# Performance work log

Measured on AMD Instinct MI355X. Metric: run time of the kernel, lower is better.

Reference implementation:

```python
import jax, jax.numpy as jnp
import numpy as np

AUDIO_IN = VIDEO_IN = TEXT_IN = 300
AH = VH = TH = 100
POST_DIM = 300
OUT_DIM = 300
BATCH = 128


def setup_inputs() -> dict:
    key = jax.random.key(0)
    ks = jax.random.split(key, 12)
    s = lambda fan_in: 1.0 / np.sqrt(fan_in)
    fusion_dim = (AH + 1) * (VH + 1) * (TH + 1)
    return {
        "audio_x": jax.random.normal(ks[0], (BATCH, AUDIO_IN), jnp.float32),
        "video_x": jax.random.normal(ks[1], (BATCH, VIDEO_IN), jnp.float32),
        "text_x": jax.random.normal(ks[2], (BATCH, TEXT_IN), jnp.float32),
        "Wa": jax.random.normal(ks[3], (AH, AUDIO_IN), jnp.float32) * s(AUDIO_IN),
        "ba": jnp.zeros((AH,), jnp.float32),
        "Wv": jax.random.normal(ks[4], (VH, VIDEO_IN), jnp.float32) * s(VIDEO_IN),
        "bv": jnp.zeros((VH,), jnp.float32),
        "Wt": jax.random.normal(ks[5], (TH, TEXT_IN), jnp.float32) * s(TEXT_IN),
        "bt": jnp.zeros((TH,), jnp.float32),
        "W1": jax.random.normal(ks[6], (POST_DIM, fusion_dim), jnp.float32) * s(fusion_dim),
        "b1": jnp.zeros((POST_DIM,), jnp.float32),
        "W2": jax.random.normal(ks[7], (OUT_DIM, POST_DIM), jnp.float32) * s(POST_DIM),
        "b2": jnp.zeros((OUT_DIM,), jnp.float32),
    }


def reference(audio_x, video_x, text_x, Wa, ba, Wv, bv, Wt, bt, W1, b1, W2, b2):
    B = audio_x.shape[0]
    audio_h = audio_x @ Wa.T + ba          # [B, AH]
    video_h = video_x @ Wv.T + bv          # [B, VH]
    text_h = text_x @ Wt.T + bt            # [B, TH]
    ones = jnp.ones((B, 1), audio_h.dtype)
    _a = jnp.concatenate([ones, audio_h], axis=1)   # [B, AH+1]
    _v = jnp.concatenate([ones, video_h], axis=1)   # [B, VH+1]
    _t = jnp.concatenate([ones, text_h], axis=1)    # [B, TH+1]
    # three-way outer product; flatten order matches torch bmm chain: (a, v, t)
    fusion = jnp.einsum('ba,bv,bt->bavt', _a, _v, _t).reshape(B, -1)
    # dropout is identity in eval mode
    h = jax.nn.relu(fusion @ W1.T + b1)
    out = jax.nn.relu(h @ W2.T + b2)
    return out
```

## Files before the change

### kernel.cpp

```cpp
#include <hip/hip_runtime.h>
#include <hip/hip_bf16.h>
#include <stdint.h>

#define NB      128
#define NH      101
#define NIN     300
#define NP      300
#define NO      300
#define K_TOT   1030301
#define NAV     10201
#define CHUNK   32
#define NCHUNKS ((K_TOT + CHUNK - 1) / CHUNK)
#define RANGES_DEFAULT 153
#define PTILES  5
#define PPAD    320
#define ASTRIDE 40
#define TSTRIDE 102

typedef __attribute__((ext_vector_type(8))) short bf16x8;
typedef __attribute__((ext_vector_type(4))) float f32x4;

static __device__ __forceinline__ unsigned short f2bf(float f) {
    union { float f; unsigned u; } x; x.f = f;
    unsigned r = x.u + 0x7fffu + ((x.u >> 16) & 1u);
    return (unsigned short)(r >> 16);
}
static __device__ __forceinline__ float bf2f(unsigned short h) {
    union { unsigned u; float f; } x; x.u = ((unsigned)h) << 16;
    return x.f;
}

__global__ __launch_bounds__(256) void proj_kernel(
    const float* __restrict__ ax, const float* __restrict__ vx, const float* __restrict__ tx,
    const float* __restrict__ Wa, const float* __restrict__ ba,
    const float* __restrict__ Wv, const float* __restrict__ bv,
    const float* __restrict__ Wt, const float* __restrict__ bt,
    float* __restrict__ Af, float* __restrict__ Vf, float* __restrict__ Tf)
{
    int g = blockIdx.x * 256 + threadIdx.x;
    if (g >= 3 * NB * NH) return;
    int mod = g / (NB * NH);
    int rem = g - mod * (NB * NH);
    int b = rem / NH, j = rem - b * NH;
    const float* x = (mod == 0) ? ax : (mod == 1) ? vx : tx;
    const float* W = (mod == 0) ? Wa : (mod == 1) ? Wv : Wt;
    const float* bi = (mod == 0) ? ba : (mod == 1) ? bv : bt;
    float val;
    if (j == 0) {
        val = 1.0f;
    } else {
        const float4* xr = (const float4*)(x + (size_t)b * NIN);
        const float4* wr = (const float4*)(W + (size_t)(j - 1) * NIN);
        float s0 = 0.f, s1 = 0.f, s2 = 0.f, s3 = 0.f;
        #pragma unroll 5
        for (int i = 0; i < NIN / 4; ++i) {
            float4 a = xr[i], w = wr[i];
            s0 += a.x * w.x; s1 += a.y * w.y; s2 += a.z * w.z; s3 += a.w * w.w;
        }
        val = (s0 + s1) + (s2 + s3) + bi[j - 1];
    }
    float* dst = (mod == 0) ? Af : (mod == 1) ? Vf : Tf;
    dst[b * NH + j] = val;
}

__global__ __launch_bounds__(256) void av_kernel(
    const float* __restrict__ Af, const float* __restrict__ Vf, const float* __restrict__ Tf,
    unsigned short* __restrict__ AVbf, unsigned short* __restrict__ Tbf)
{
    int g = blockIdx.x * 256 + threadIdx.x;
    if (g < NB * TSTRIDE) {
        int b = g / TSTRIDE, j = g - b * TSTRIDE;
        Tbf[g] = (j < NH) ? f2bf(Tf[b * NH + j]) : (unsigned short)0;
    }
    if (g < NAV * NB) {
        int av = g >> 7, b = g & 127;
        int a = av / NH, v = av - a * NH;
        AVbf[g] = f2bf(Af[b * NH + a] * Vf[b * NH + v]);
    }
}

__global__ __launch_bounds__(256) void fusion_gemm_kernel(
    const float* __restrict__ W1, const unsigned short* __restrict__ AVbf,
    const unsigned short* __restrict__ Tbf, float* __restrict__ partial, int cpr)
{
    __shared__ unsigned short Tl[NB * TSTRIDE];
    __shared__ unsigned short Al[NB * ASTRIDE];
    __shared__ unsigned short Wl[64 * ASTRIDE];

    const int tid   = threadIdx.x;
    const int ptile = blockIdx.x;
    const int rng   = blockIdx.y;
    const int wave  = tid >> 6;
    const int lane  = tid & 63;
    const int ln15  = lane & 15;
    const int quad  = lane >> 4;

    {
        const unsigned* src = (const unsigned*)Tbf;
        unsigned* dst = (unsigned*)Tl;
        for (int i = tid; i < NB * TSTRIDE / 2; i += 256) dst[i] = src[i];
    }

    const int c0 = rng * cpr;
    const int c1 = min(c0 + cpr, NCHUNKS);

    const int kk   = tid & 31;
    const int bg   = (tid >> 5) << 4;
    const int wrow = tid >> 5;

    f32x4 acc[8];
    #pragma unroll
    for (int i = 0; i < 8; ++i) acc[i] = (f32x4){0.f, 0.f, 0.f, 0.f};

    float    wreg[8];
    unsigned avp[8];
    unsigned tt = 0;
    bool     valid = true;

    __syncthreads();

    auto issue_loads = [&](int c) {
        unsigned kg = (unsigned)c * CHUNK + (unsigned)kk;
        valid = (kg < K_TOT);
        unsigned kc = valid ? kg : (unsigned)(K_TOT - 1);
        #pragma unroll
        for (int it = 0; it < 8; ++it) {
            int pr = ptile * 64 + wrow + it * 8;
            if (pr > NP - 1) pr = NP - 1;
            wreg[it] = W1[(size_t)pr * K_TOT + kc];
        }
        unsigned av = kc / 101u;
        tt = kc - av * 101u;
        const unsigned* avsrc = (const unsigned*)(AVbf + (size_t)av * NB + bg);
        #pragma unroll
        for (int j = 0; j < 8; ++j) avp[j] = avsrc[j];
    };

    if (c0 < c1) issue_loads(c0);

    for (int c = c0; c < c1; ++c) {
        #pragma unroll
        for (int it = 0; it < 8; ++it)
            Wl[(wrow + it * 8) * ASTRIDE + kk] = f2bf(wreg[it]);
        #pragma unroll
        for (int j2 = 0; j2 < 8; ++j2) {
            unsigned pk = avp[j2];
            int b0 = bg + j2 * 2;
            float a0 = bf2f((unsigned short)(pk & 0xffffu));
            float a1 = bf2f((unsigned short)(pk >> 16));
            float t0 = bf2f(Tl[b0 * TSTRIDE + tt]);
            float t1 = bf2f(Tl[(b0 + 1) * TSTRIDE + tt]);
            Al[b0 * ASTRIDE + kk]       = valid ? f2bf(a0 * t0) : (unsigned short)0;
            Al[(b0 + 1) * ASTRIDE + kk] = valid ? f2bf(a1 * t1) : (unsigned short)0;
        }
        __syncthreads();
        if (c + 1 < c1) issue_loads(c + 1);
        bf16x8 bfrag = *(const bf16x8*)&Wl[(wave * 16 + ln15) * ASTRIDE + quad * 8];
        #pragma unroll
        for (int bt = 0; bt < 8; ++bt) {
            bf16x8 afrag = *(const bf16x8*)&Al[(bt * 16 + ln15) * ASTRIDE + quad * 8];
            acc[bt] = __builtin_amdgcn_mfma_f32_16x16x32_bf16(afrag, bfrag, acc[bt], 0, 0, 0);
        }
        __syncthreads();
    }

    const int p = ptile * 64 + wave * 16 + ln15;
    #pragma unroll
    for (int bt = 0; bt < 8; ++bt) {
        #pragma unroll
        for (int rg = 0; rg < 4; ++rg) {
            int b = bt * 16 + quad * 4 + rg;
            partial[((size_t)rng * NB + b) * PPAD + p] = acc[bt][rg];
        }
    }
}

__global__ __launch_bounds__(256) void reduce_kernel(
    const float* __restrict__ partial, const float* __restrict__ b1,
    float* __restrict__ h, int R)
{
    int g = blockIdx.x * 256 + threadIdx.x;
    if (g >= NB * NP) return;
    int b = g / NP, p = g - b * NP;
    float s = b1[p];
    const float* src = partial + (size_t)b * PPAD + p;
    for (int r = 0; r < R; ++r) s += src[(size_t)r * NB * PPAD];
    h[b * NP + p] = fmaxf(s, 0.f);
}

__global__ __launch_bounds__(256) void gemm2_kernel(
    const float* __restrict__ h, const float* __restrict__ W2,
    const float* __restrict__ b2, float* __restrict__ out)
{
    int g = blockIdx.x * 256 + threadIdx.x;
    if (g >= NB * NO) return;
    int b = g / NO, o = g - b * NO;
    const float4* hr = (const float4*)(h + (size_t)b * NP);
    const float4* wr = (const float4*)(W2 + (size_t)o * NP);
    float s0 = 0.f, s1 = 0.f, s2 = 0.f, s3 = 0.f;
    #pragma unroll 5
    for (int i = 0; i < NP / 4; ++i) {
        float4 a = hr[i], w = wr[i];
        s0 += a.x * w.x; s1 += a.y * w.y; s2 += a.z * w.z; s3 += a.w * w.w;
    }
    out[g] = fmaxf((s0 + s1) + (s2 + s3) + b2[o], 0.f);
}

extern "C" void kernel_launch(void* const* d_in, const int* in_sizes, int n_in,
                              void* d_out, int out_size, void* d_ws, size_t ws_size,
                              hipStream_t stream) {
    const float* ax = (const float*)d_in[0];
    const float* vx = (const float*)d_in[1];
    const float* tx = (const float*)d_in[2];
    const float* Wa = (const float*)d_in[3];
    const float* ba = (const float*)d_in[4];
    const float* Wv = (const float*)d_in[5];
    const float* bv = (const float*)d_in[6];
    const float* Wt = (const float*)d_in[7];
    const float* bt = (const float*)d_in[8];
    const float* W1 = (const float*)d_in[9];
    const float* b1 = (const float*)d_in[10];
    const float* W2 = (const float*)d_in[11];
    const float* b2 = (const float*)d_in[12];
    float* out = (float*)d_out;

    char* ws = (char*)d_ws;
    size_t off = 0;
    float* Af = (float*)(ws + off); off += (size_t)NB * NH * 4;
    float* Vf = (float*)(ws + off); off += (size_t)NB * NH * 4;
    float* Tf = (float*)(ws + off); off += (size_t)NB * NH * 4;
    float* h  = (float*)(ws + off); off += (size_t)NB * NP * 4;
    unsigned short* Tbf  = (unsigned short*)(ws + off); off += (size_t)NB * TSTRIDE * 2;
    unsigned short* AVbf = (unsigned short*)(ws + off); off += (size_t)NAV * NB * 2;
    size_t fixed = off;
    const size_t per_range = (size_t)NB * PPAD * 4;
    int R = RANGES_DEFAULT;
    if (ws_size < fixed + (size_t)R * per_range) {
        size_t avail = (ws_size > fixed) ? (ws_size - fixed) : per_range;
        R = (int)(avail / per_range);
        if (R < 1) R = 1;
    }
    float* partial = (float*)(ws + fixed);
    int cpr = (NCHUNKS + R - 1) / R;

    proj_kernel<<<(3 * NB * NH + 255) / 256, 256, 0, stream>>>(
        ax, vx, tx, Wa, ba, Wv, bv, Wt, bt, Af, Vf, Tf);
    av_kernel<<<(NAV * NB + 255) / 256, 256, 0, stream>>>(Af, Vf, Tf, AVbf, Tbf);
    fusion_gemm_kernel<<<dim3(PTILES, R), 256, 0, stream>>>(W1, AVbf, Tbf, partial, cpr);
    reduce_kernel<<<(NB * NP + 255) / 256, 256, 0, stream>>>(partial, b1, h, R);
    gemm2_kernel<<<(NB * NO + 255) / 256, 256, 0, stream>>>(h, W2, b2, out);
}
```

Measured before the change: 1.762 ms.

## Restructure fusion GEMM to iterate over av pairs with register-built MFMA fragments

The fusion GEMM now splits K by (a,v) pairs instead of flat 32-wide chunks. Each wave loads its W1 row segment of 101 t-values directly into registers as float4 and converts with a packed bf16 instruction. The A fragment is built on the fly from the LDS-resident T table scaled by the av scalar, so the per-chunk LDS staging of W and A and both barriers go away. The cost is padding waste in the final 5-element slice of each segment, misaligned float4 loads of W1 since rows are 101 floats apart, and the workspace-size fallback being dropped.

```diff
diff --git a/kernel.cpp b/kernel.cpp
--- a/kernel.cpp
+++ b/kernel.cpp
@@ -9,13 +9,11 @@
 #define NO      300
 #define K_TOT   1030301
 #define NAV     10201
-#define CHUNK   32
-#define NCHUNKS ((K_TOT + CHUNK - 1) / CHUNK)
-#define RANGES_DEFAULT 153
+#define TSTR    104
+#define PPAD    320
 #define PTILES  5
-#define PPAD    320
-#define ASTRIDE 40
-#define TSTRIDE 102
+#define RANGES  153
+#define APR     ((NAV + RANGES - 1) / RANGES)
 
 typedef __attribute__((ext_vector_type(8))) short bf16x8;
 typedef __attribute__((ext_vector_type(4))) float f32x4;
@@ -28,6 +26,17 @@
 static __device__ __forceinline__ float bf2f(unsigned short h) {
     union { unsigned u; float f; } x; x.u = ((unsigned)h) << 16;
     return x.f;
+}
+static __device__ __forceinline__ float u2f(uint32_t u) {
+    union { uint32_t u; float f; } x; x.u = u; return x.f;
+}
+static __device__ __forceinline__ uint32_t pk2(float x, float y) {
+    uint32_t r;
+    asm("v_cvt_pk_bf16_f32 %0, %1, %2" : "=v"(r) : "v"(x), "v"(y));
+    return r;
+}
+static __device__ __forceinline__ float4 loadf4(const float* q) {
+    float4 v; __builtin_memcpy(&v, q, 16); return v;
 }
 
 __global__ __launch_bounds__(256) void proj_kernel(
@@ -68,8 +77,8 @@
     unsigned short* __restrict__ AVbf, unsigned short* __restrict__ Tbf)
 {
     int g = blockIdx.x * 256 + threadIdx.x;
-    if (g < NB * TSTRIDE) {
-        int b = g / TSTRIDE, j = g - b * TSTRIDE;
+    if (g < NB * TSTR) {
+        int b = g / TSTR, j = g - b * TSTR;
         Tbf[g] = (j < NH) ? f2bf(Tf[b * NH + j]) : (unsigned short)0;
     }
     if (g < NAV * NB) {
@@ -79,89 +88,114 @@
     }
 }
 
-__global__ __launch_bounds__(256) void fusion_gemm_kernel(
+__global__ __launch_bounds__(256, 3) void fusion_gemm_kernel(
     const float* __restrict__ W1, const unsigned short* __restrict__ AVbf,
-    const unsigned short* __restrict__ Tbf, float* __restrict__ partial, int cpr)
-{
-    __shared__ unsigned short Tl[NB * TSTRIDE];
-    __shared__ unsigned short Al[NB * ASTRIDE];
-    __shared__ unsigned short Wl[64 * ASTRIDE];
-
-    const int tid   = threadIdx.x;
+    const unsigned short* __restrict__ Tbf, float* __restrict__ partial, int apr)
+{
+    __shared__ __align__(16) unsigned short Tl[NB * TSTR];
+    __shared__ __align__(16) unsigned short AVl[(APR + 1) * NB];
+
+    const int tid  = threadIdx.x;
     const int ptile = blockIdx.x;
-    const int rng   = blockIdx.y;
-    const int wave  = tid >> 6;
-    const int lane  = tid & 63;
-    const int ln15  = lane & 15;
-    const int quad  = lane >> 4;
+    const int rng  = blockIdx.y;
+    const int wave = tid >> 6;
+    const int lane = tid & 63;
+    const int ln15 = lane & 15;
+    const int quad = lane >> 4;
+
+    const int av0 = rng * apr;
+    const int av_end = min(av0 + apr, NAV);
+    const int nav = av_end - av0;
 
     {
-        const unsigned* src = (const unsigned*)Tbf;
-        unsigned* dst = (unsigned*)Tl;
-        for (int i = tid; i < NB * TSTRIDE / 2; i += 256) dst[i] = src[i];
-    }
-
-    const int c0 = rng * cpr;
-    const int c1 = min(c0 + cpr, NCHUNKS);
-
-    const int kk   = tid & 31;
-    const int bg   = (tid >> 5) << 4;
-    const int wrow = tid >> 5;
+        const uint32_t* src = (const uint32_t*)Tbf;
+        uint32_t* dst = (uint32_t*)Tl;
+        #pragma unroll
+        for (int i = 0; i < (NB * TSTR / 2) / 256; ++i)
+            dst[i * 256 + tid] = src[i * 256 + tid];
+        if (nav > 0) {
+            const uint32_t* s2 = (const uint32_t*)(AVbf + (size_t)av0 * NB);
+            uint32_t* d2 = (uint32_t*)AVl;
+            const int ndw = nav * (NB / 2);
+            for (int i = tid; i < ndw; i += 256) d2[i] = s2[i];
+        }
+    }
+    __syncthreads();
+
+    int prow = ptile * 64 + wave * 16 + ln15;
+    if (prow > NP - 1) prow = NP - 1;
+    const float* wrow = W1 + (size_t)prow * K_TOT;
 
     f32x4 acc[8];
     #pragma unroll
     for (int i = 0; i < 8; ++i) acc[i] = (f32x4){0.f, 0.f, 0.f, 0.f};
 
-    float    wreg[8];
-    unsigned avp[8];
-    unsigned tt = 0;
-    bool     valid = true;
-
-    __syncthreads();
-
-    auto issue_loads = [&](int c) {
-        unsigned kg = (unsigned)c * CHUNK + (unsigned)kk;
-        valid = (kg < K_TOT);
-        unsigned kc = valid ? kg : (unsigned)(K_TOT - 1);
-        #pragma unroll
-        for (int it = 0; it < 8; ++it) {
-            int pr = ptile * 64 + wrow + it * 8;
-            if (pr > NP - 1) pr = NP - 1;
-            wreg[it] = W1[(size_t)pr * K_TOT + kc];
-        }
-        unsigned av = kc / 101u;
-        tt = kc - av * 101u;
-        const unsigned* avsrc = (const unsigned*)(AVbf + (size_t)av * NB + bg);
-        #pragma unroll
-        for (int j = 0; j < 8; ++j) avp[j] = avsrc[j];
-    };
-
-    if (c0 < c1) issue_loads(c0);
-
-    for (int c = c0; c < c1; ++c) {
-        #pragma unroll
-        for (int it = 0; it < 8; ++it)
-            Wl[(wrow + it * 8) * ASTRIDE + kk] = f2bf(wreg[it]);
-        #pragma unroll
-        for (int j2 = 0; j2 < 8; ++j2) {
-            unsigned pk = avp[j2];
-            int b0 = bg + j2 * 2;
-            float a0 = bf2f((unsigned short)(pk & 0xffffu));
-            float a1 = bf2f((unsigned short)(pk >> 16));
-            float t0 = bf2f(Tl[b0 * TSTRIDE + tt]);
-            float t1 = bf2f(Tl[(b0 + 1) * TSTRIDE + tt]);
-            Al[b0 * ASTRIDE + kk]       = valid ? f2bf(a0 * t0) : (unsigned short)0;
-            Al[(b0 + 1) * ASTRIDE + kk] = valid ? f2bf(a1 * t1) : (unsigned short)0;
-        }
-        __syncthreads();
-        if (c + 1 < c1) issue_loads(c + 1);
-        bf16x8 bfrag = *(const bf16x8*)&Wl[(wave * 16 + ln15) * ASTRIDE + quad * 8];
-        #pragma unroll
-        for (int bt = 0; bt < 8; ++bt) {
-            bf16x8 afrag = *(const bf16x8*)&Al[(bt * 16 + ln15) * ASTRIDE + quad * 8];
-            acc[bt] = __builtin_amdgcn_mfma_f32_16x16x32_bf16(afrag, bfrag, acc[bt], 0, 0, 0);
-        }
-        __syncthreads();
+    #pragma unroll 1
+    for (int a = 0; a < nav; ++a) {
+        const float* wbase = wrow + (size_t)(av0 + a) * 101;
+
+        float4 wq[6];
+        #pragma unroll
+        for (int s = 0; s < 3; ++s) {
+            const float* q = wbase + s * 32 + quad * 8;
+            wq[s * 2]     = loadf4(q);
+            wq[s * 2 + 1] = loadf4(q + 4);
+        }
+        float w3[5];
+        #pragma unroll
+        for (int j = 0; j < 5; ++j) w3[j] = wbase[96 + j];
+
+        float avf[8];
+        #pragma unroll
+        for (int bt = 0; bt < 8; ++bt)
+            avf[bt] = bf2f(AVl[a * NB + bt * 16 + ln15]);
+
+        #pragma unroll
+        for (int s = 0; s < 3; ++s) {
+            union { bf16x8 v; uint32_t u[4]; } bf;
+            bf.u[0] = pk2(wq[s * 2].x,     wq[s * 2].y);
+            bf.u[1] = pk2(wq[s * 2].z,     wq[s * 2].w);
+            bf.u[2] = pk2(wq[s * 2 + 1].x, wq[s * 2 + 1].y);
+            bf.u[3] = pk2(wq[s * 2 + 1].z, wq[s * 2 + 1].w);
+            #pragma unroll
+            for (int bt = 0; bt < 8; ++bt) {
+                const uint4 t4 = *(const uint4*)&Tl[(bt * 16 + ln15) * TSTR + s * 32 + quad * 8];
+                const float s0 = avf[bt];
+                union { bf16x8 v; uint32_t u[4]; } af;
+                af.u[0] = pk2(s0 * u2f(t4.x << 16), s0 * u2f(t4.x & 0xffff0000u));
+                af.u[1] = pk2(s0 * u2f(t4.y << 16), s0 * u2f(t4.y & 0xffff0000u));
+                af.u[2] = pk2(s0 * u2f(t4.z << 16), s0 * u2f(t4.z & 0xffff0000u));
+                af.u[3] = pk2(s0 * u2f(t4.w << 16), s0 * u2f(t4.w & 0xffff0000u));
+                acc[bt] = __builtin_amdgcn_mfma_f32_16x16x32_bf16(af.v, bf.v, acc[bt], 0, 0, 0);
+            }
+        }
+
+        {
+            union { bf16x8 v; uint32_t u[4]; } bf;
+            if (quad == 0) {
+                bf.u[0] = pk2(w3[0], w3[1]);
+                bf.u[1] = pk2(w3[2], w3[3]);
+                bf.u[2] = pk2(w3[4], 0.f);
+                bf.u[3] = 0u;
+            } else {
+                bf.u[0] = 0u; bf.u[1] = 0u; bf.u[2] = 0u; bf.u[3] = 0u;
+            }
+            #pragma unroll
+            for (int bt = 0; bt < 8; ++bt) {
+                union { bf16x8 v; uint32_t u[4]; } af;
+                if (quad == 0) {
+                    const uint4 t4 = *(const uint4*)&Tl[(bt * 16 + ln15) * TSTR + 96];
+                    const float s0 = avf[bt];
+                    af.u[0] = pk2(s0 * u2f(t4.x << 16), s0 * u2f(t4.x & 0xffff0000u));
+                    af.u[1] = pk2(s0 * u2f(t4.y << 16), s0 * u2f(t4.y & 0xffff0000u));
+                    af.u[2] = pk2(s0 * u2f(t4.z << 16), s0 * u2f(t4.z & 0xffff0000u));
+                    af.u[3] = pk2(s0 * u2f(t4.w << 16), s0 * u2f(t4.w & 0xffff0000u));
+                } else {
+                    af.u[0] = 0u; af.u[1] = 0u; af.u[2] = 0u; af.u[3] = 0u;
+                }
+                acc[bt] = __builtin_amdgcn_mfma_f32_16x16x32_bf16(af.v, bf.v, acc[bt], 0, 0, 0);
+            }
+        }
     }
 
     const int p = ptile * 64 + wave * 16 + ln15;
@@ -230,23 +264,17 @@
     float* Vf = (float*)(ws + off); off += (size_t)NB * NH * 4;
     float* Tf = (float*)(ws + off); off += (size_t)NB * NH * 4;
     float* h  = (float*)(ws + off); off += (size_t)NB * NP * 4;
-    unsigned short* Tbf  = (unsigned short*)(ws + off); off += (size_t)NB * TSTRIDE * 2;
+    unsigned short* Tbf  = (unsigned short*)(ws + off); off += (size_t)NB * TSTR * 2;
     unsigned short* AVbf = (unsigned short*)(ws + off); off += (size_t)NAV * NB * 2;
-    size_t fixed = off;
-    const size_t per_range = (size_t)NB * PPAD * 4;
-    int R = RANGES_DEFAULT;
-    if (ws_size < fixed + (size_t)R * per_range) {
-        size_t avail = (ws_size > fixed) ? (ws_size - fixed) : per_range;
-        R = (int)(avail / per_range);
-        if (R < 1) R = 1;
-    }
-    float* partial = (float*)(ws + fixed);
-    int cpr = (NCHUNKS + R - 1) / R;
+    float* partial = (float*)(ws + off);
+
+    const int R = RANGES;
+    const int apr = APR;
 
     proj_kernel<<<(3 * NB * NH + 255) / 256, 256, 0, stream>>>(
         ax, vx, tx, Wa, ba, Wv, bv, Wt, bt, Af, Vf, Tf);
     av_kernel<<<(NAV * NB + 255) / 256, 256, 0, stream>>>(Af, Vf, Tf, AVbf, Tbf);
-    fusion_gemm_kernel<<<dim3(PTILES, R), 256, 0, stream>>>(W1, AVbf, Tbf, partial, cpr);
+    fusion_gemm_kernel<<<dim3(PTILES, R), 256, 0, stream>>>(W1, AVbf, Tbf, partial, apr);
     reduce_kernel<<<(NB * NP + 255) / 256, 256, 0, stream>>>(partial, b1, h, R);
     gemm2_kernel<<<(NB * NO + 255) / 256, 256, 0, stream>>>(h, W2, b2, out);
 }
```

Measured after the change: 1.720 ms. 2.4% less time.
